# Optimization experiments

Hardware: AMD Instinct MI355X
Metric: run time of the kernel (lower is better)

Reference implementation:

```python
import jax, jax.numpy as jnp
import numpy as np

REG_MAX = 16
BOX_W = 7.5
OBJ_W = 1.0
TOPK = 10
EPS = 1e-7


def dfl_decode(x, reg_max):
    # x: [B, 4*reg_max, N] -> expected value of per-side distribution -> [B, N, 4] (xyxy)
    B, C, N = x.shape
    x = x.reshape(B, 4, reg_max, N)
    p = jax.nn.softmax(x, axis=2)
    proj = jnp.arange(reg_max, dtype=x.dtype)
    return jnp.einsum('bkrn,r->bnk', p, proj)


def bbox_ciou(b1, b2):
    # b1: [B,N,1,4], b2: [B,1,M,4], xyxy -> [B,N,M]
    x11, y11, x12, y12 = b1[..., 0], b1[..., 1], b1[..., 2], b1[..., 3]
    x21, y21, x22, y22 = b2[..., 0], b2[..., 1], b2[..., 2], b2[..., 3]
    w1, h1 = x12 - x11, y12 - y11
    w2, h2 = x22 - x21, y22 - y21
    iw = jnp.clip(jnp.minimum(x12, x22) - jnp.maximum(x11, x21), 0.0)
    ih = jnp.clip(jnp.minimum(y12, y22) - jnp.maximum(y11, y21), 0.0)
    inter = iw * ih
    union = w1 * h1 + w2 * h2 - inter + EPS
    iou = inter / union
    cw = jnp.maximum(x12, x22) - jnp.minimum(x11, x21)
    ch = jnp.maximum(y12, y22) - jnp.minimum(y11, y21)
    c2 = cw * cw + ch * ch + EPS
    rho2 = ((x21 + x22 - x11 - x12) ** 2 + (y21 + y22 - y11 - y12) ** 2) * 0.25
    v = (4.0 / (np.pi ** 2)) * (jnp.arctan(w2 / (h2 + EPS)) - jnp.arctan(w1 / (h1 + EPS))) ** 2
    alpha = jax.lax.stop_gradient(v / (v - iou + 1.0 + EPS))
    return iou - rho2 / c2 - alpha * v


def setup_inputs() -> dict:
    key = jax.random.key(0)
    k1, k2, k3, k4 = jax.random.split(key, 4)
    B, N, M = 8, 34000, 64
    boxes = jax.random.normal(k1, (B, 4 * REG_MAX, N), dtype=jnp.float32)
    scores = jax.random.normal(k2, (B, N), dtype=jnp.float32)
    # GT boxes: valid xyxy in roughly the same [0, reg_max) range as decoded preds
    xy = jax.random.uniform(k3, (B, M, 2), dtype=jnp.float32) * 11.0
    wh = jax.random.uniform(k4, (B, M, 2), dtype=jnp.float32) * 4.0 + 0.5
    targets = jnp.concatenate([xy, xy + wh], axis=-1)
    return {'boxes': boxes, 'scores': scores, 'targets': targets}


def reference(boxes, scores, targets):
    B, N = scores.shape
    M = targets.shape[1]
    pb = dfl_decode(boxes, REG_MAX)                     # [B,N,4]
    ciou = bbox_ciou(pb[:, :, None, :], targets[:, None, :, :])  # [B,N,M]
    k = min(TOPK, N)
    topv, topi = jax.lax.top_k(jnp.swapaxes(ciou, 1, 2), k)      # [B,M,k] over anchors
    valid = topv > 0.0
    vals = jnp.where(valid, topv, 0.0)

    def per_batch(idx, val, vld):
        flat_i = idx.reshape(-1)
        iou_t = jnp.zeros((N,), val.dtype).at[flat_i].max(val.reshape(-1))
        pos = jnp.zeros((N,), bool).at[flat_i].max(vld.reshape(-1))
        return iou_t, pos

    iou_target, pos = jax.vmap(per_batch)(topi, vals, valid)     # [B,N]
    posf = pos.astype(iou_target.dtype)
    npos = posf.sum(axis=1)
    box_per = jnp.where(npos > 0,
                        ((1.0 - iou_target) * posf).sum(axis=1) / jnp.maximum(npos, 1.0),
                        0.0)
    box_loss = box_per.sum()
    # BCEWithLogits (mean over anchors), summed over batch
    bce = jnp.maximum(scores, 0.0) - scores * iou_target + jnp.log1p(jnp.exp(-jnp.abs(scores)))
    obj_loss = bce.mean(axis=1).sum()
    total = (BOX_W * box_loss + OBJ_W * obj_loss) / B
    return total, box_loss, obj_loss
```

## Files before the change

### kernel.cpp

```cpp
#include <hip/hip_runtime.h>
#include <math.h>

#define BQ 8
#define MQ 64
#define REGMAX 16
#define KTOP 10
#define EPSQ 1e-7f
#define MBUF 1344

__device__ __forceinline__ float frcp(float x) { return __builtin_amdgcn_rcpf(x); }

#define ST_BYTES 256

__device__ __forceinline__ float dfl_side(const float* __restrict__ p, size_t Ns) {
  float x0 = p[0];
  float x1 = p[Ns];
  float x2 = p[2 * Ns];
  float x3 = p[3 * Ns];
  float x4 = p[4 * Ns];
  float x5 = p[5 * Ns];
  float x6 = p[6 * Ns];
  float x7 = p[7 * Ns];
  float x8 = p[8 * Ns];
  float x9 = p[9 * Ns];
  float x10 = p[10 * Ns];
  float x11 = p[11 * Ns];
  float x12 = p[12 * Ns];
  float x13 = p[13 * Ns];
  float x14 = p[14 * Ns];
  float x15 = p[15 * Ns];
  float mx = fmaxf(fmaxf(fmaxf(fmaxf(x0, x1), fmaxf(x2, x3)),
                         fmaxf(fmaxf(x4, x5), fmaxf(x6, x7))),
                   fmaxf(fmaxf(fmaxf(x8, x9), fmaxf(x10, x11)),
                         fmaxf(fmaxf(x12, x13), fmaxf(x14, x15))));
  float s = 0.f, ws = 0.f, e;
  e = __expf(x0 - mx); s += e;
  e = __expf(x1 - mx); s += e; ws += 1.f * e;
  e = __expf(x2 - mx); s += e; ws += 2.f * e;
  e = __expf(x3 - mx); s += e; ws += 3.f * e;
  e = __expf(x4 - mx); s += e; ws += 4.f * e;
  e = __expf(x5 - mx); s += e; ws += 5.f * e;
  e = __expf(x6 - mx); s += e; ws += 6.f * e;
  e = __expf(x7 - mx); s += e; ws += 7.f * e;
  e = __expf(x8 - mx); s += e; ws += 8.f * e;
  e = __expf(x9 - mx); s += e; ws += 9.f * e;
  e = __expf(x10 - mx); s += e; ws += 10.f * e;
  e = __expf(x11 - mx); s += e; ws += 11.f * e;
  e = __expf(x12 - mx); s += e; ws += 12.f * e;
  e = __expf(x13 - mx); s += e; ws += 13.f * e;
  e = __expf(x14 - mx); s += e; ws += 14.f * e;
  e = __expf(x15 - mx); s += e; ws += 15.f * e;
  return ws * frcp(s);
}

__global__ __launch_bounds__(256) void decode_topk_kernel(
    const float* __restrict__ boxes, const float* __restrict__ scores,
    const float* __restrict__ targets, unsigned int* __restrict__ iou_bits,
    uint2* __restrict__ cand, float* __restrict__ acc, int N, int bpb) {
  const int tid = threadIdx.x;
  const int b = blockIdx.x / bpb;
  const int blk = blockIdx.x - b * bpb;
  const int a0 = blk * 256;
  const int w = tid >> 6;
  const int l = tid & 63;

  __shared__ float4 s_sv[256];
  __shared__ float s_at[256];
  __shared__ int s_ix[256];
  __shared__ float s_hv[4 * MQ * KTOP];
  __shared__ int s_hi[4 * MQ * KTOP];
  __shared__ uint2 s_mg[MQ * KTOP];
  __shared__ int s_cnt;
  __shared__ float s_bce;
  if (tid == 0) { s_cnt = 0; s_bce = 0.f; }
  __syncthreads();

  const int n = a0 + tid;
  float bce0 = 0.f;
  if (n < N) {
    const size_t i = (size_t)b * N + n;
    iou_bits[i] = 0u;
    float sc = scores[i];
    bce0 = fmaxf(sc, 0.f) + log1pf(__expf(-fabsf(sc)));
    const size_t Ns = (size_t)N;
    const float* base = boxes + (size_t)(b * 64) * Ns + n;
    float ev0 = dfl_side(base, Ns);
    float ev1 = dfl_side(base + 16 * Ns, Ns);
    float ev2 = dfl_side(base + 32 * Ns, Ns);
    float ev3 = dfl_side(base + 48 * Ns, Ns);
    float w1 = ev2 - ev0, h1 = ev3 - ev1;
    if (w1 > 0.f && h1 > 0.f) {
      int slot = atomicAdd(&s_cnt, 1);
      s_sv[slot] = make_float4(ev0, ev1, ev2, ev3);
      s_at[slot] = atanf(w1 * frcp(h1 + EPSQ));
      s_ix[slot] = n;
    }
  }
#pragma unroll
  for (int d = 1; d < 64; d <<= 1) bce0 += __shfl_xor(bce0, d, 64);
  if (l == 0) atomicAdd(&s_bce, bce0);
  __syncthreads();
  const int nsurv = s_cnt;
  if (tid == 0) atomicAdd(&acc[b * 4 + 2], s_bce);

  const float4 t = ((const float4*)targets)[b * MQ + l];
  const float x21 = t.x, y21 = t.y, x22 = t.z, y22 = t.w;
  const float w2 = x22 - x21, h2 = y22 - y21;
  const float atan_t = atanf(w2 * frcp(h2 + EPSQ));
  const float area2 = w2 * h2, sumx2 = x21 + x22, sumy2 = y21 + y22;
  const float CPI = 4.0f / (float)(M_PI * M_PI);

  float hv0 = 0.f, hv1 = 0.f, hv2 = 0.f, hv3 = 0.f, hv4 = 0.f;
  float hv5 = 0.f, hv6 = 0.f, hv7 = 0.f, hv8 = 0.f, hv9 = 0.f;
  int hi0 = 0, hi1 = 0, hi2 = 0, hi3 = 0, hi4 = 0;
  int hi5 = 0, hi6 = 0, hi7 = 0, hi8 = 0, hi9 = 0;

  const int qlen = (nsurv + 3) >> 2;
  const int j0 = w * qlen;
  const int j1 = min(nsurv, j0 + qlen);
  for (int j = j0; j < j1; ++j) {
    float4 p = s_sv[j];
    float pa = s_at[j];
    int ixj = s_ix[j];
    float x11 = p.x, y11 = p.y, x12 = p.z, y12 = p.w;
    float w1 = x12 - x11, h1 = y12 - y11;
    float iw = fmaxf(fminf(x12, x22) - fmaxf(x11, x21), 0.f);
    float ih = fmaxf(fminf(y12, y22) - fmaxf(y11, y21), 0.f);
    float inter = iw * ih;
    float uni = w1 * h1 + area2 - inter + EPSQ;
    float iou = inter * frcp(uni);
    float cw = fmaxf(x12, x22) - fminf(x11, x21);
    float ch = fmaxf(y12, y22) - fminf(y11, y21);
    float c2 = cw * cw + ch * ch + EPSQ;
    float dx = sumx2 - x11 - x12;
    float dy = sumy2 - y11 - y12;
    float rho2 = (dx * dx + dy * dy) * 0.25f;
    float da = atan_t - pa;
    float v = CPI * da * da;
    float alpha = v * frcp(v - iou + 1.f + EPSQ);
    float ciou = iou - rho2 * frcp(c2) - alpha * v;
    if (ciou > hv9) {
      float cv = ciou;
      int ci = ixj;
#define INS(vk, ik)                         \
  {                                         \
    bool gt = cv > vk;                      \
    float tv_ = vk; int ti_ = ik;           \
    vk = gt ? cv : vk; ik = gt ? ci : ik;   \
    cv = gt ? tv_ : cv; ci = gt ? ti_ : ci; \
  }
      INS(hv0, hi0) INS(hv1, hi1) INS(hv2, hi2) INS(hv3, hi3) INS(hv4, hi4)
      INS(hv5, hi5) INS(hv6, hi6) INS(hv7, hi7) INS(hv8, hi8) INS(hv9, hi9)
#undef INS
    }
  }
  const int hb = (w * MQ + l) * KTOP;
  s_hv[hb + 0] = hv0; s_hi[hb + 0] = hi0;
  s_hv[hb + 1] = hv1; s_hi[hb + 1] = hi1;
  s_hv[hb + 2] = hv2; s_hi[hb + 2] = hi2;
  s_hv[hb + 3] = hv3; s_hi[hb + 3] = hi3;
  s_hv[hb + 4] = hv4; s_hi[hb + 4] = hi4;
  s_hv[hb + 5] = hv5; s_hi[hb + 5] = hi5;
  s_hv[hb + 6] = hv6; s_hi[hb + 6] = hi6;
  s_hv[hb + 7] = hv7; s_hi[hb + 7] = hi7;
  s_hv[hb + 8] = hv8; s_hi[hb + 8] = hi8;
  s_hv[hb + 9] = hv9; s_hi[hb + 9] = hi9;
  __syncthreads();

  if (w == 0) {
    const int m = l;
    int p0 = 0, p1 = 0, p2 = 0, p3 = 0;
    for (int r = 0; r < KTOP; ++r) {
      float c0 = s_hv[(0 * MQ + m) * KTOP + p0];
      float c1 = s_hv[(1 * MQ + m) * KTOP + p1];
      float c2m = s_hv[(2 * MQ + m) * KTOP + p2];
      float c3 = s_hv[(3 * MQ + m) * KTOP + p3];
      float best = c0; int bw = 0;
      if (c1 > best) { best = c1; bw = 1; }
      if (c2m > best) { best = c2m; bw = 2; }
      if (c3 > best) { best = c3; bw = 3; }
      int psel = (bw == 0) ? p0 : (bw == 1) ? p1 : (bw == 2) ? p2 : p3;
      int bidx = s_hi[(bw * MQ + m) * KTOP + psel];
      s_mg[m * KTOP + r] = make_uint2(__float_as_uint(best), (unsigned)bidx);
      if (bw == 0) p0 = min(p0 + 1, KTOP - 1);
      else if (bw == 1) p1 = min(p1 + 1, KTOP - 1);
      else if (bw == 2) p2 = min(p2 + 1, KTOP - 1);
      else p3 = min(p3 + 1, KTOP - 1);
    }
  }
  __syncthreads();
  uint2* obase = cand + (size_t)(b * bpb + blk) * (MQ * KTOP);
  for (int sl = tid; sl < MQ * KTOP; sl += 256) obase[sl] = s_mg[sl];
}

__device__ __forceinline__ void select_top10(
    float* s_bv, int* s_bi, float* s_winv, int* s_wini,
    int* s_cnt, int c, int tid) {
  if (tid < 64) {
    for (int r = 0; r < KTOP; ++r) {
      float bv = 0.f;
      int bs = 0xffff;
      for (int sl = tid; sl < c; sl += 64) {
        float v = s_bv[sl];
        if (v > bv) { bv = v; bs = sl; }
      }
      unsigned long long key =
          ((unsigned long long)__float_as_uint(bv) << 32) | (unsigned int)bs;
#pragma unroll
      for (int d = 1; d < 64; d <<= 1) {
        unsigned long long o = __shfl_xor(key, d, 64);
        if (o > key) key = o;
      }
      if (tid == 0) {
        float wv = __uint_as_float((unsigned int)(key >> 32));
        int ws = (int)(key & 0xffffu);
        s_winv[r] = wv;
        if (wv > 0.f && ws != 0xffff) {
          s_wini[r] = s_bi[ws];
          s_bv[ws] = 0.f;
        } else {
          s_wini[r] = 0;
        }
      }
    }
    if (tid < KTOP) { s_bv[tid] = s_winv[tid]; s_bi[tid] = s_wini[tid]; }
    if (tid == 0) *s_cnt = KTOP;
  }
}

__global__ __launch_bounds__(256) void merge_kernel(
    const uint2* __restrict__ cand, const float* __restrict__ scores,
    unsigned int* __restrict__ iou_bits, float* __restrict__ acc,
    int N, int bpb) {
  const int bm = blockIdx.x;
  const int b = bm >> 6;
  const int m = bm & 63;
  const int tid = threadIdx.x;
  const int NC = bpb * KTOP;

  __shared__ float s_bv[MBUF];
  __shared__ int s_bi[MBUF];
  __shared__ float s_winv[KTOP];
  __shared__ int s_wini[KTOP];
  __shared__ int s_cnt;
  if (tid == 0) s_cnt = 0;
  __syncthreads();

  for (int k2 = tid; k2 < NC; k2 += 256) {
    int blkk = k2 / KTOP;
    int r = k2 - blkk * KTOP;
    uint2 e = cand[((size_t)(b * bpb + blkk) * MQ + m) * KTOP + r];
    float v = __uint_as_float(e.x);
    if (v > 0.f) {
      int slot = atomicAdd(&s_cnt, 1);
      s_bv[slot] = v;
      s_bi[slot] = (int)e.y;
    }
  }
  __syncthreads();
  int c = s_cnt;
  __syncthreads();
  if (c > KTOP) {
    select_top10(s_bv, s_bi, s_winv, s_wini, &s_cnt, c, tid);
    __syncthreads();
    c = KTOP;
  }
  if (tid < KTOP && tid < c) {
    float v = s_bv[tid];
    if (v > 0.f) {
      int ix = s_bi[tid];
      unsigned int vb = __float_as_uint(v);
      unsigned int old = atomicMax(&iou_bits[(size_t)b * N + ix], vb);
      if (old < vb) {
        float vold = __uint_as_float(old);
        bool was = (old != 0u);
        atomicAdd(&acc[b * 4 + 0], was ? (vold - v) : (1.f - v));
        if (!was) atomicAdd(&acc[b * 4 + 1], 1.f);
        atomicAdd(&acc[b * 4 + 2], -scores[(size_t)b * N + ix] * (v - vold));
      }
    }
  }
}

__global__ void finalize_kernel(const float* __restrict__ acc,
                                float* __restrict__ out, int N) {
  if (threadIdx.x == 0 && blockIdx.x == 0) {
    float box = 0.f, obj = 0.f;
    for (int bb = 0; bb < BQ; ++bb) {
      float sb = acc[bb * 4 + 0];
      float np = acc[bb * 4 + 1];
      float sc = acc[bb * 4 + 2];
      box += (np > 0.f) ? sb / fmaxf(np, 1.f) : 0.f;
      obj += sc / (float)N;
    }
    out[0] = (7.5f * box + obj) / (float)BQ;
    out[1] = box;
    out[2] = obj;
  }
}

extern "C" void kernel_launch(void* const* d_in, const int* in_sizes, int n_in,
                              void* d_out, int out_size, void* d_ws, size_t ws_size,
                              hipStream_t stream) {
  const float* boxes = (const float*)d_in[0];
  const float* scores = (const float*)d_in[1];
  const float* targets = (const float*)d_in[2];
  float* out = (float*)d_out;
  const int N = in_sizes[1] / BQ;

  const int bpb = (N + 255) / 256;

  char* ws = (char*)d_ws;
  size_t cand_bytes = (size_t)BQ * bpb * MQ * KTOP * sizeof(uint2);
  size_t iou_bytes = (size_t)BQ * N * sizeof(unsigned int);

  uint2* cand = (uint2*)ws;                    ws += cand_bytes;
  unsigned int* iou_bits = (unsigned int*)ws;  ws += iou_bytes;
  float* state = (float*)ws;

  hipMemsetAsync(state, 0, ST_BYTES, stream);

  decode_topk_kernel<<<BQ * bpb, 256, 0, stream>>>(boxes, scores, targets,
                                                   iou_bits, cand, state, N, bpb);
  merge_kernel<<<BQ * MQ, 256, 0, stream>>>(cand, scores, iou_bits, state, N, bpb);
  finalize_kernel<<<1, 64, 0, stream>>>(state, out, N);
}
```

Before: 142.1 us.

## Process two anchors per thread, transpose candidate layout, fuse finalize into merge

Each decode thread now handles two adjacent anchors using float2 loads, so a block covers 512 anchors and the number of per-block candidate lists is halved. Candidates are stored with a per-(batch, target) contiguous layout so the merge kernel reads them with coalesced loads. The memset and finalize launches are removed: per-block BCE and per-(b,m) partial sums go to workspace, and the last merge block, found with an atomic counter, reduces them and writes the outputs. This adds register pressure and shared memory in the decode kernel and relies on correct fence and counter ordering.

```diff
diff --git a/kernel.cpp b/kernel.cpp
--- a/kernel.cpp
+++ b/kernel.cpp
@@ -6,11 +6,10 @@
 #define REGMAX 16
 #define KTOP 10
 #define EPSQ 1e-7f
-#define MBUF 1344
+#define APB 512
+#define MBUF 1024
 
 __device__ __forceinline__ float frcp(float x) { return __builtin_amdgcn_rcpf(x); }
-
-#define ST_BYTES 256
 
 __device__ __forceinline__ float dfl_side(const float* __restrict__ p, size_t Ns) {
   float x0 = p[0];
@@ -53,47 +52,136 @@
   return ws * frcp(s);
 }
 
+__device__ __forceinline__ float2 dfl_side2(const float* __restrict__ p, size_t Ns) {
+  float2 x0 = *(const float2*)(p);
+  float2 x1 = *(const float2*)(p + Ns);
+  float2 x2 = *(const float2*)(p + 2 * Ns);
+  float2 x3 = *(const float2*)(p + 3 * Ns);
+  float2 x4 = *(const float2*)(p + 4 * Ns);
+  float2 x5 = *(const float2*)(p + 5 * Ns);
+  float2 x6 = *(const float2*)(p + 6 * Ns);
+  float2 x7 = *(const float2*)(p + 7 * Ns);
+  float2 x8 = *(const float2*)(p + 8 * Ns);
+  float2 x9 = *(const float2*)(p + 9 * Ns);
+  float2 x10 = *(const float2*)(p + 10 * Ns);
+  float2 x11 = *(const float2*)(p + 11 * Ns);
+  float2 x12 = *(const float2*)(p + 12 * Ns);
+  float2 x13 = *(const float2*)(p + 13 * Ns);
+  float2 x14 = *(const float2*)(p + 14 * Ns);
+  float2 x15 = *(const float2*)(p + 15 * Ns);
+  float mxa = fmaxf(fmaxf(fmaxf(fmaxf(x0.x, x1.x), fmaxf(x2.x, x3.x)),
+                          fmaxf(fmaxf(x4.x, x5.x), fmaxf(x6.x, x7.x))),
+                    fmaxf(fmaxf(fmaxf(x8.x, x9.x), fmaxf(x10.x, x11.x)),
+                          fmaxf(fmaxf(x12.x, x13.x), fmaxf(x14.x, x15.x))));
+  float mxb = fmaxf(fmaxf(fmaxf(fmaxf(x0.y, x1.y), fmaxf(x2.y, x3.y)),
+                          fmaxf(fmaxf(x4.y, x5.y), fmaxf(x6.y, x7.y))),
+                    fmaxf(fmaxf(fmaxf(x8.y, x9.y), fmaxf(x10.y, x11.y)),
+                          fmaxf(fmaxf(x12.y, x13.y), fmaxf(x14.y, x15.y))));
+  float sa = 0.f, wa = 0.f, sb = 0.f, wb = 0.f, e;
+  e = __expf(x0.x - mxa); sa += e;
+  e = __expf(x0.y - mxb); sb += e;
+  e = __expf(x1.x - mxa); sa += e; wa += 1.f * e;
+  e = __expf(x1.y - mxb); sb += e; wb += 1.f * e;
+  e = __expf(x2.x - mxa); sa += e; wa += 2.f * e;
+  e = __expf(x2.y - mxb); sb += e; wb += 2.f * e;
+  e = __expf(x3.x - mxa); sa += e; wa += 3.f * e;
+  e = __expf(x3.y - mxb); sb += e; wb += 3.f * e;
+  e = __expf(x4.x - mxa); sa += e; wa += 4.f * e;
+  e = __expf(x4.y - mxb); sb += e; wb += 4.f * e;
+  e = __expf(x5.x - mxa); sa += e; wa += 5.f * e;
+  e = __expf(x5.y - mxb); sb += e; wb += 5.f * e;
+  e = __expf(x6.x - mxa); sa += e; wa += 6.f * e;
+  e = __expf(x6.y - mxb); sb += e; wb += 6.f * e;
+  e = __expf(x7.x - mxa); sa += e; wa += 7.f * e;
+  e = __expf(x7.y - mxb); sb += e; wb += 7.f * e;
+  e = __expf(x8.x - mxa); sa += e; wa += 8.f * e;
+  e = __expf(x8.y - mxb); sb += e; wb += 8.f * e;
+  e = __expf(x9.x - mxa); sa += e; wa += 9.f * e;
+  e = __expf(x9.y - mxb); sb += e; wb += 9.f * e;
+  e = __expf(x10.x - mxa); sa += e; wa += 10.f * e;
+  e = __expf(x10.y - mxb); sb += e; wb += 10.f * e;
+  e = __expf(x11.x - mxa); sa += e; wa += 11.f * e;
+  e = __expf(x11.y - mxb); sb += e; wb += 11.f * e;
+  e = __expf(x12.x - mxa); sa += e; wa += 12.f * e;
+  e = __expf(x12.y - mxb); sb += e; wb += 12.f * e;
+  e = __expf(x13.x - mxa); sa += e; wa += 13.f * e;
+  e = __expf(x13.y - mxb); sb += e; wb += 13.f * e;
+  e = __expf(x14.x - mxa); sa += e; wa += 14.f * e;
+  e = __expf(x14.y - mxb); sb += e; wb += 14.f * e;
+  e = __expf(x15.x - mxa); sa += e; wa += 15.f * e;
+  e = __expf(x15.y - mxb); sb += e; wb += 15.f * e;
+  return make_float2(wa * frcp(sa), wb * frcp(sb));
+}
+
 __global__ __launch_bounds__(256) void decode_topk_kernel(
     const float* __restrict__ boxes, const float* __restrict__ scores,
     const float* __restrict__ targets, unsigned int* __restrict__ iou_bits,
-    uint2* __restrict__ cand, float* __restrict__ acc, int N, int bpb) {
+    uint2* __restrict__ cand, float* __restrict__ bcePartial,
+    unsigned int* __restrict__ ctr, int N, int bpb) {
   const int tid = threadIdx.x;
   const int b = blockIdx.x / bpb;
   const int blk = blockIdx.x - b * bpb;
-  const int a0 = blk * 256;
+  const int a0 = blk * APB;
   const int w = tid >> 6;
   const int l = tid & 63;
 
-  __shared__ float4 s_sv[256];
-  __shared__ float s_at[256];
-  __shared__ int s_ix[256];
+  __shared__ float4 s_sv[APB];
+  __shared__ float s_at[APB];
+  __shared__ int s_ix[APB];
   __shared__ float s_hv[4 * MQ * KTOP];
   __shared__ int s_hi[4 * MQ * KTOP];
   __shared__ uint2 s_mg[MQ * KTOP];
   __shared__ int s_cnt;
   __shared__ float s_bce;
   if (tid == 0) { s_cnt = 0; s_bce = 0.f; }
-  __syncthreads();
-
-  const int n = a0 + tid;
+  if (blockIdx.x == 0 && tid == 0) *ctr = 0u;
+  __syncthreads();
+
+  const int n0 = a0 + 2 * tid;
   float bce0 = 0.f;
-  if (n < N) {
-    const size_t i = (size_t)b * N + n;
-    iou_bits[i] = 0u;
-    float sc = scores[i];
-    bce0 = fmaxf(sc, 0.f) + log1pf(__expf(-fabsf(sc)));
+  if (n0 < N) {
+    const size_t i = (size_t)b * N + n0;
     const size_t Ns = (size_t)N;
-    const float* base = boxes + (size_t)(b * 64) * Ns + n;
-    float ev0 = dfl_side(base, Ns);
-    float ev1 = dfl_side(base + 16 * Ns, Ns);
-    float ev2 = dfl_side(base + 32 * Ns, Ns);
-    float ev3 = dfl_side(base + 48 * Ns, Ns);
-    float w1 = ev2 - ev0, h1 = ev3 - ev1;
-    if (w1 > 0.f && h1 > 0.f) {
-      int slot = atomicAdd(&s_cnt, 1);
-      s_sv[slot] = make_float4(ev0, ev1, ev2, ev3);
-      s_at[slot] = atanf(w1 * frcp(h1 + EPSQ));
-      s_ix[slot] = n;
+    const float* base = boxes + (size_t)(b * 64) * Ns + n0;
+    if (n0 + 1 < N) {
+      iou_bits[i] = 0u;
+      iou_bits[i + 1] = 0u;
+      float2 sc = *(const float2*)(scores + i);
+      bce0 = fmaxf(sc.x, 0.f) + log1pf(__expf(-fabsf(sc.x))) +
+             fmaxf(sc.y, 0.f) + log1pf(__expf(-fabsf(sc.y)));
+      float2 ev0 = dfl_side2(base, Ns);
+      float2 ev1 = dfl_side2(base + 16 * Ns, Ns);
+      float2 ev2 = dfl_side2(base + 32 * Ns, Ns);
+      float2 ev3 = dfl_side2(base + 48 * Ns, Ns);
+      float w1 = ev2.x - ev0.x, h1 = ev3.x - ev1.x;
+      if (w1 > 0.f && h1 > 0.f) {
+        int slot = atomicAdd(&s_cnt, 1);
+        s_sv[slot] = make_float4(ev0.x, ev1.x, ev2.x, ev3.x);
+        s_at[slot] = atanf(w1 * frcp(h1 + EPSQ));
+        s_ix[slot] = n0;
+      }
+      float w1b = ev2.y - ev0.y, h1b = ev3.y - ev1.y;
+      if (w1b > 0.f && h1b > 0.f) {
+        int slot = atomicAdd(&s_cnt, 1);
+        s_sv[slot] = make_float4(ev0.y, ev1.y, ev2.y, ev3.y);
+        s_at[slot] = atanf(w1b * frcp(h1b + EPSQ));
+        s_ix[slot] = n0 + 1;
+      }
+    } else {
+      iou_bits[i] = 0u;
+      float sc = scores[i];
+      bce0 = fmaxf(sc, 0.f) + log1pf(__expf(-fabsf(sc)));
+      float ev0 = dfl_side(base, Ns);
+      float ev1 = dfl_side(base + 16 * Ns, Ns);
+      float ev2 = dfl_side(base + 32 * Ns, Ns);
+      float ev3 = dfl_side(base + 48 * Ns, Ns);
+      float w1 = ev2 - ev0, h1 = ev3 - ev1;
+      if (w1 > 0.f && h1 > 0.f) {
+        int slot = atomicAdd(&s_cnt, 1);
+        s_sv[slot] = make_float4(ev0, ev1, ev2, ev3);
+        s_at[slot] = atanf(w1 * frcp(h1 + EPSQ));
+        s_ix[slot] = n0;
+      }
     }
   }
 #pragma unroll
@@ -101,7 +189,7 @@
   if (l == 0) atomicAdd(&s_bce, bce0);
   __syncthreads();
   const int nsurv = s_cnt;
-  if (tid == 0) atomicAdd(&acc[b * 4 + 2], s_bce);
+  if (tid == 0) bcePartial[blockIdx.x] = s_bce;
 
   const float4 t = ((const float4*)targets)[b * MQ + l];
   const float x21 = t.x, y21 = t.y, x22 = t.z, y22 = t.w;
@@ -189,8 +277,11 @@
     }
   }
   __syncthreads();
-  uint2* obase = cand + (size_t)(b * bpb + blk) * (MQ * KTOP);
-  for (int sl = tid; sl < MQ * KTOP; sl += 256) obase[sl] = s_mg[sl];
+  for (int sl = tid; sl < MQ * KTOP; sl += 256) {
+    int m = sl / KTOP;
+    int r = sl - m * KTOP;
+    cand[((size_t)(b * MQ + m) * bpb + blk) * KTOP + r] = s_mg[sl];
+  }
 }
 
 __device__ __forceinline__ void select_top10(
@@ -230,11 +321,11 @@
 
 __global__ __launch_bounds__(256) void merge_kernel(
     const uint2* __restrict__ cand, const float* __restrict__ scores,
-    unsigned int* __restrict__ iou_bits, float* __restrict__ acc,
-    int N, int bpb) {
+    unsigned int* __restrict__ iou_bits, const float* __restrict__ bcePartial,
+    float* __restrict__ mergePartial, unsigned int* __restrict__ ctr,
+    float* __restrict__ out, int N, int bpb) {
   const int bm = blockIdx.x;
   const int b = bm >> 6;
-  const int m = bm & 63;
   const int tid = threadIdx.x;
   const int NC = bpb * KTOP;
 
@@ -243,13 +334,16 @@
   __shared__ float s_winv[KTOP];
   __shared__ int s_wini[KTOP];
   __shared__ int s_cnt;
+  __shared__ float s_d[3];
+  __shared__ int s_last;
+  __shared__ float s_box[BQ], s_obj[BQ];
   if (tid == 0) s_cnt = 0;
-  __syncthreads();
-
+  if (tid < 3) s_d[tid] = 0.f;
+  __syncthreads();
+
+  const uint2* cbase = cand + (size_t)bm * NC;
   for (int k2 = tid; k2 < NC; k2 += 256) {
-    int blkk = k2 / KTOP;
-    int r = k2 - blkk * KTOP;
-    uint2 e = cand[((size_t)(b * bpb + blkk) * MQ + m) * KTOP + r];
+    uint2 e = cbase[k2];
     float v = __uint_as_float(e.x);
     if (v > 0.f) {
       int slot = atomicAdd(&s_cnt, 1);
@@ -274,28 +368,46 @@
       if (old < vb) {
         float vold = __uint_as_float(old);
         bool was = (old != 0u);
-        atomicAdd(&acc[b * 4 + 0], was ? (vold - v) : (1.f - v));
-        if (!was) atomicAdd(&acc[b * 4 + 1], 1.f);
-        atomicAdd(&acc[b * 4 + 2], -scores[(size_t)b * N + ix] * (v - vold));
-      }
-    }
-  }
-}
-
-__global__ void finalize_kernel(const float* __restrict__ acc,
-                                float* __restrict__ out, int N) {
-  if (threadIdx.x == 0 && blockIdx.x == 0) {
-    float box = 0.f, obj = 0.f;
-    for (int bb = 0; bb < BQ; ++bb) {
-      float sb = acc[bb * 4 + 0];
-      float np = acc[bb * 4 + 1];
-      float sc = acc[bb * 4 + 2];
-      box += (np > 0.f) ? sb / fmaxf(np, 1.f) : 0.f;
-      obj += sc / (float)N;
-    }
-    out[0] = (7.5f * box + obj) / (float)BQ;
-    out[1] = box;
-    out[2] = obj;
+        atomicAdd(&s_d[0], was ? (vold - v) : (1.f - v));
+        if (!was) atomicAdd(&s_d[1], 1.f);
+        atomicAdd(&s_d[2], -scores[(size_t)b * N + ix] * (v - vold));
+      }
+    }
+  }
+  __syncthreads();
+  if (tid == 0) {
+    float4* mp = (float4*)(mergePartial + (size_t)bm * 4);
+    *mp = make_float4(s_d[0], s_d[1], s_d[2], 0.f);
+    __threadfence();
+    unsigned int done = atomicAdd(ctr, 1u);
+    s_last = (done == (unsigned)(gridDim.x - 1)) ? 1 : 0;
+  }
+  __syncthreads();
+  if (s_last) {
+    __threadfence();
+    if (tid < BQ) {
+      const int bb = tid;
+      volatile const float* mp = mergePartial;
+      float sbox = 0.f, snp = 0.f, sbce = 0.f;
+      for (int mm = 0; mm < MQ; ++mm) {
+        int idx = (bb * MQ + mm) * 4;
+        sbox += mp[idx];
+        snp += mp[idx + 1];
+        sbce += mp[idx + 2];
+      }
+      volatile const float* bp = bcePartial;
+      for (int k2 = 0; k2 < bpb; ++k2) sbce += bp[bb * bpb + k2];
+      s_box[bb] = (snp > 0.f) ? sbox / fmaxf(snp, 1.f) : 0.f;
+      s_obj[bb] = sbce / (float)N;
+    }
+    __syncthreads();
+    if (tid == 0) {
+      float box = 0.f, obj = 0.f;
+      for (int bb = 0; bb < BQ; ++bb) { box += s_box[bb]; obj += s_obj[bb]; }
+      out[0] = (7.5f * box + obj) / (float)BQ;
+      out[1] = box;
+      out[2] = obj;
+    }
   }
 }
 
@@ -308,20 +420,23 @@
   float* out = (float*)d_out;
   const int N = in_sizes[1] / BQ;
 
-  const int bpb = (N + 255) / 256;
+  const int bpb = (N + APB - 1) / APB;
+  const int nblk = BQ * bpb;
 
   char* ws = (char*)d_ws;
-  size_t cand_bytes = (size_t)BQ * bpb * MQ * KTOP * sizeof(uint2);
+  size_t cand_bytes = (size_t)BQ * MQ * bpb * KTOP * sizeof(uint2);
   size_t iou_bytes = (size_t)BQ * N * sizeof(unsigned int);
+  size_t bce_bytes = (((size_t)nblk * sizeof(float)) + 255) & ~(size_t)255;
+  size_t mp_bytes = (size_t)BQ * MQ * 4 * sizeof(float);
 
   uint2* cand = (uint2*)ws;                    ws += cand_bytes;
   unsigned int* iou_bits = (unsigned int*)ws;  ws += iou_bytes;
-  float* state = (float*)ws;
-
-  hipMemsetAsync(state, 0, ST_BYTES, stream);
-
-  decode_topk_kernel<<<BQ * bpb, 256, 0, stream>>>(boxes, scores, targets,
-                                                   iou_bits, cand, state, N, bpb);
-  merge_kernel<<<BQ * MQ, 256, 0, stream>>>(cand, scores, iou_bits, state, N, bpb);
-  finalize_kernel<<<1, 64, 0, stream>>>(state, out, N);
-}
+  float* bcePartial = (float*)ws;              ws += bce_bytes;
+  float* mergePartial = (float*)ws;            ws += mp_bytes;
+  unsigned int* ctr = (unsigned int*)ws;
+
+  decode_topk_kernel<<<nblk, 256, 0, stream>>>(boxes, scores, targets,
+                                               iou_bits, cand, bcePartial, ctr, N, bpb);
+  merge_kernel<<<BQ * MQ, 256, 0, stream>>>(cand, scores, iou_bits, bcePartial,
+                                            mergePartial, ctr, out, N, bpb);
+}
```

Result: slower. 164.3 us (+15.6%).
